# Kernel optimization log

Measured on AMD Instinct MI355X. Metric: run time of the kernel, lower is better.

## Reference

```python
import jax, jax.numpy as jnp
import numpy as np
import math

H, KVH, D = 15, 5, 64  # heads, kv heads, head_dim
ROPE_BASE = 10000.0
NEG = -1e9


def _rope_cos_sin(position_ids):
    # position_ids: [B, S] int -> cos/sin [B, 1, S, D]
    inv_freq = 1.0 / (ROPE_BASE ** (jnp.arange(0, D, 2, dtype=jnp.float32) / D))  # [D/2]
    freqs = position_ids.astype(jnp.float32)[..., None] * inv_freq  # [B, S, D/2]
    emb = jnp.concatenate([freqs, freqs], axis=-1)  # [B, S, D]
    return jnp.cos(emb)[:, None], jnp.sin(emb)[:, None]


def _rotate_half(x):
    x1, x2 = x[..., : D // 2], x[..., D // 2 :]
    return jnp.concatenate([-x2, x1], axis=-1)


def setup_inputs() -> dict:
    key = jax.random.key(0)
    ks = jax.random.split(key, 5)
    B, S, E = 1, 4096, 960
    hidden_states = jax.random.normal(ks[0], (B, S, E), dtype=jnp.float32)
    Wq = jax.random.normal(ks[1], (E, E), dtype=jnp.float32) * 0.02
    Wk = jax.random.normal(ks[2], (KVH * D, E), dtype=jnp.float32) * 0.02
    Wv = jax.random.normal(ks[3], (KVH * D, E), dtype=jnp.float32) * 0.02
    Wo = jax.random.normal(ks[4], (E, E), dtype=jnp.float32) * 0.02
    causal = jnp.tril(jnp.ones((S, S), dtype=bool))
    attention_mask = jnp.where(causal, 0.0, NEG).astype(jnp.float32)[None, None]  # [1,1,S,S]
    position_ids = jnp.arange(S, dtype=jnp.int64 if jax.config.jax_enable_x64 else jnp.int32)[None]
    return {
        "hidden_states": hidden_states,
        "Wq": Wq,
        "Wk": Wk,
        "Wv": Wv,
        "Wo": Wo,
        "attention_mask": attention_mask,
        "position_ids": position_ids,
    }


def reference(hidden_states, Wq, Wk, Wv, Wo, attention_mask, position_ids):
    B, S, E = hidden_states.shape
    groups = H // KVH
    # projections (bias-free Linear: x @ W.T)
    q = (hidden_states @ Wq.T).reshape(B, S, H, D).transpose(0, 2, 1, 3)      # [B,H,S,D]
    k = (hidden_states @ Wk.T).reshape(B, S, KVH, D).transpose(0, 2, 1, 3)    # [B,KVH,S,D]
    v = (hidden_states @ Wv.T).reshape(B, S, KVH, D).transpose(0, 2, 1, 3)    # [B,KVH,S,D]
    cos, sin = _rope_cos_sin(position_ids)  # [B,1,S,D]
    q = q * cos + _rotate_half(q) * sin
    k = k * cos + _rotate_half(k) * sin
    # GQA: repeat_interleave over the head axis
    k = jnp.repeat(k, groups, axis=1)  # [B,H,S,D]
    v = jnp.repeat(v, groups, axis=1)  # [B,H,S,D]
    scores = jnp.einsum("bhqd,bhkd->bhqk", q, k) / math.sqrt(D) + attention_mask
    probs = jax.nn.softmax(scores.astype(jnp.float32), axis=-1).astype(q.dtype)
    out = jnp.einsum("bhqk,bhkd->bhqd", probs, v)  # [B,H,S,D]
    out = out.transpose(0, 2, 1, 3).reshape(B, S, E)
    return out @ Wo.T
```

## Files before the change

kernel.cpp:

```cpp
#include <hip/hip_runtime.h>
#include <hip/hip_bf16.h>

typedef __hip_bfloat16 bf16;
typedef short bf16x8 __attribute__((ext_vector_type(8)));
typedef short bf16x4 __attribute__((ext_vector_type(4)));
typedef float f32x4 __attribute__((ext_vector_type(4)));

static constexpr int S_LEN = 4096;
static constexpr int EMB   = 960;
static constexpr int NH    = 15;
static constexpr int NKVH  = 5;
static constexpr int KV_E  = NKVH * 64;

__device__ __forceinline__ float scrub(float x, float lim) {
  return fminf(fmaxf(x, -lim), lim);
}

__device__ __forceinline__ short f2bf(float x) {
  bf16 h = __float2bfloat16(x);
  short s;
  __builtin_memcpy(&s, &h, 2);
  return s;
}

__device__ __forceinline__ void stage16(const bf16* g, bf16* l) {
  __builtin_amdgcn_global_load_lds(
      (const __attribute__((address_space(1))) void*)g,
      (__attribute__((address_space(3))) void*)l, 16, 0, 0);
}

__global__ void cvt5_kernel(const float* s0, const float* s1, const float* s2,
                            const float* s3, const float* s4,
                            bf16* d0, bf16* d1, bf16* d2, bf16* d3, bf16* d4,
                            int e0, int e1, int e2, int e3, int e4) {
  int i = blockIdx.x * blockDim.x + threadIdx.x;
  const float* s;
  bf16* d;
  int base;
  if (i < e0)      { s = s0; d = d0; base = 0;  }
  else if (i < e1) { s = s1; d = d1; base = e0; }
  else if (i < e2) { s = s2; d = d2; base = e1; }
  else if (i < e3) { s = s3; d = d3; base = e2; }
  else if (i < e4) { s = s4; d = d4; base = e3; }
  else return;
  int k = i - base;
  const float4* sp = (const float4*)s + (size_t)k * 2;
  float4 a = sp[0], b = sp[1];
  bf16x8 r;
  r[0] = f2bf(a.x); r[1] = f2bf(a.y); r[2] = f2bf(a.z); r[3] = f2bf(a.w);
  r[4] = f2bf(b.x); r[5] = f2bf(b.y); r[6] = f2bf(b.z); r[7] = f2bf(b.w);
  *(bf16x8*)((short*)d + (size_t)k * 8) = r;
}

__global__ void zero_kernel(float* __restrict__ p, int n4) {
  int i = blockIdx.x * blockDim.x + threadIdx.x;
  if (i < n4) ((float4*)p)[i] = (float4){0.f, 0.f, 0.f, 0.f};
}

template <typename EPI>
__device__ __forceinline__ void gemm_core(
    const bf16* __restrict__ A, const bf16* __restrict__ W,
    int m0, int n0, int K, bf16* At0, bf16* At1, bf16* Bt0, bf16* Bt1,
    EPI&& epilogue) {
  const int lane = threadIdx.x & 63;
  const int wave = threadIdx.x >> 6;
  const int quad = lane >> 4;
  const int c16  = lane & 15;
  const int wm = wave >> 1, wn = wave & 1;
  const int srow = lane >> 2;
  const int sch  = lane & 3;
  const int NIT  = K / 32;
  bf16* At[2] = {At0, At1};
  bf16* Bt[2] = {Bt0, Bt1};

  auto stage = [&](int b, int k0) {
#pragma unroll
    for (int t = 0; t < 2; t++) {
      int j = wave * 2 + t;
      stage16(A + (size_t)(m0 + j * 16 + srow) * K + k0 + sch * 8,
              At[b] + j * 512);
      stage16(W + (size_t)(n0 + j * 16 + srow) * K + k0 + sch * 8,
              Bt[b] + j * 512);
    }
  };

  f32x4 acc[4][4];
#pragma unroll
  for (int i = 0; i < 4; i++)
#pragma unroll
    for (int j = 0; j < 4; j++) acc[i][j] = (f32x4){0.f, 0.f, 0.f, 0.f};

  stage(0, 0);
  __syncthreads();

  for (int it = 0; it < NIT; ++it) {
    if (it + 1 < NIT) stage((it + 1) & 1, (it + 1) * 32);
    const char* ab = (const char*)At[it & 1];
    const char* bb = (const char*)Bt[it & 1];
    bf16x8 af[4], bfr[4];
#pragma unroll
    for (int i = 0; i < 4; i++)
      af[i] = *(const bf16x8*)(ab + (wm * 64 + i * 16 + c16) * 64 + quad * 16);
#pragma unroll
    for (int j = 0; j < 4; j++)
      bfr[j] = *(const bf16x8*)(bb + (wn * 64 + j * 16 + c16) * 64 + quad * 16);
#pragma unroll
    for (int i = 0; i < 4; i++)
#pragma unroll
      for (int j = 0; j < 4; j++)
        acc[i][j] = __builtin_amdgcn_mfma_f32_16x16x32_bf16(af[i], bfr[j],
                                                            acc[i][j], 0, 0, 0);
    __syncthreads();
  }
  epilogue(acc, m0, n0, wm, wn, quad, c16);
}

__global__ __launch_bounds__(256) void gemm_qkv_kernel(
    const bf16* __restrict__ A, const bf16* __restrict__ Wcat,
    bf16* __restrict__ Qb, bf16* __restrict__ Kbf, bf16* __restrict__ VTb,
    int M, int K) {
  __shared__ __align__(16) bf16 At[2][128 * 32];
  __shared__ __align__(16) bf16 Bt[2][128 * 32];
  const int m0 = blockIdx.x * 128;
  const int n0 = blockIdx.y * 128;
  gemm_core(A, Wcat, m0, n0, K, At[0], At[1], Bt[0], Bt[1],
            [&](f32x4 (&acc)[4][4], int m0_, int n0_, int wm, int wn,
                int quad, int c16) {
#pragma unroll
              for (int i = 0; i < 4; i++)
#pragma unroll
                for (int j = 0; j < 4; j++) {
                  int scol = n0_ + wn * 64 + j * 16;
                  if (scol >= 1600) continue;
                  int colg = scol + c16;
                  int row0 = m0_ + wm * 64 + i * 16 + quad * 4;
                  if (scol < 960) {
#pragma unroll
                    for (int r = 0; r < 4; r++)
                      Qb[(size_t)(row0 + r) * EMB + colg] =
                          __float2bfloat16(scrub(acc[i][j][r], 3e4f));
                  } else if (scol < 1280) {
#pragma unroll
                    for (int r = 0; r < 4; r++)
                      Kbf[(size_t)(row0 + r) * KV_E + (colg - 960)] =
                          __float2bfloat16(scrub(acc[i][j][r], 3e4f));
                  } else {
                    bf16x4 v;
#pragma unroll
                    for (int r = 0; r < 4; r++)
                      v[r] = f2bf(scrub(acc[i][j][r], 3e4f));
                    int t0 = m0_ + wm * 64;
                    int nl = quad * 16 + (i >> 1) * 8 + (i & 1) * 4;
                    *(bf16x4*)((short*)VTb + (size_t)(colg - 1280) * S_LEN +
                               t0 + nl) = v;
                  }
                }
            });
}

__global__ __launch_bounds__(256) void gemm_out_kernel(
    const bf16* __restrict__ A, const bf16* __restrict__ W,
    float* __restrict__ C, int M, int N, int K) {
  __shared__ __align__(16) bf16 At[2][128 * 32];
  __shared__ __align__(16) bf16 Bt[2][128 * 32];
  const int m0 = blockIdx.x * 128;
  const int n0 = blockIdx.y * 128;
  gemm_core(A, W, m0, n0, K, At[0], At[1], Bt[0], Bt[1],
            [&](f32x4 (&acc)[4][4], int m0_, int n0_, int wm, int wn,
                int quad, int c16) {
#pragma unroll
              for (int i = 0; i < 4; i++)
#pragma unroll
                for (int j = 0; j < 4; j++) {
                  int scol = n0_ + wn * 64 + j * 16;
                  if (scol >= EMB) continue;
                  int col = scol + c16;
                  int row0 = m0_ + wm * 64 + i * 16 + quad * 4;
#pragma unroll
                  for (int r = 0; r < 4; r++)
                    C[(size_t)(row0 + r) * EMB + col] =
                        scrub(acc[i][j][r], 3e4f);
                }
            });
}

__global__ void rope2_kernel(bf16* __restrict__ Qb, bf16* __restrict__ Kb,
                             const int* __restrict__ pos_ids) {
  int tid = blockIdx.x * blockDim.x + threadIdx.x;
  if (tid >= S_LEN * (NH + NKVH) * 32) return;
  int d  = tid & 31;
  int hh = (tid >> 5) % (NH + NKVH);
  int s  = tid / ((NH + NKVH) * 32);
  bf16* buf;
  size_t idx;
  float scale;
  if (hh < NH) {
    buf = Qb; idx = (size_t)s * EMB + hh * 64 + d; scale = 0.125f;
  } else {
    buf = Kb; idx = (size_t)s * KV_E + (hh - NH) * 64 + d; scale = 1.0f;
  }
  float x = __bfloat162float(buf[idx]);
  float y = __bfloat162float(buf[idx + 32]);
  float f = (float)pos_ids[s] * expf((float)d * -0.28782313662425572f);
  float sf, cf;
  sincosf(f, &sf, &cf);
  buf[idx]      = __float2bfloat16(scrub((x * cf - y * sf) * scale, 3e4f));
  buf[idx + 32] = __float2bfloat16(scrub((y * cf + x * sf) * scale, 3e4f));
}

__global__ __launch_bounds__(256, 5) void flash_kernel(
    const bf16* __restrict__ Q, const bf16* __restrict__ Kb,
    const bf16* __restrict__ VT, float* __restrict__ Oacc,
    float* __restrict__ Lacc) {
  __shared__ __align__(16) bf16 Kt[2][64 * 64];
  __shared__ __align__(16) bf16 Vt[2][64 * 64];

  const int xq = (int)(gridDim.x - 1) - (int)blockIdx.x;
  const int c  = blockIdx.z;
  if (c > (xq >> 4)) return;

  const int lane = threadIdx.x & 63;
  const int wv   = threadIdx.x >> 6;
  const int quad = lane >> 4;
  const int c16  = lane & 15;
  const int h    = blockIdx.y;
  const int kvh  = h / 3;
  const int qb   = xq * 64;
  const int qw   = qb + wv * 16;
  const int qcol = qw + c16;
  const int it0   = c * 16;
  const int itend = min(it0 + 16, xq + 1);

  const int rsub = lane >> 3;
  const int gch  = (lane & 7) ^ rsub;
  const int rm   = c16 & 7;
  const int ko0  = (quad ^ rm) * 16;

  const bf16* qrow = Q + (size_t)qcol * EMB + h * 64 + quad * 8;
  const bf16x8 aq0 = *(const bf16x8*)qrow;
  const bf16x8 aq1 = *(const bf16x8*)(qrow + 32);

  bf16x4 ones4;
#pragma unroll
  for (int j = 0; j < 4; j++) ones4[j] = (short)0x3F80;

  f32x4 o[4];
#pragma unroll
  for (int n = 0; n < 4; n++) o[n] = (f32x4){0.f, 0.f, 0.f, 0.f};
  f32x4 os = (f32x4){0.f, 0.f, 0.f, 0.f};

  auto stage = [&](int b, int it) {
    const int kbase = it * 64;
#pragma unroll
    for (int t = 0; t < 2; t++) {
      int i = wv * 2 + t;
      int r = i * 8 + rsub;
      stage16(Kb + (size_t)(kbase + r) * KV_E + kvh * 64 + gch * 8,
              &Kt[b][i * 512]);
      stage16(VT + (size_t)(kvh * 64 + r) * S_LEN + kbase + gch * 8,
              &Vt[b][i * 512]);
    }
  };

  stage(0, it0);
  __syncthreads();

  for (int it = it0; it < itend; ++it) {
    if (it + 1 < itend) stage((it + 1) & 1, it + 1);

    const int kbase = it * 64;
    const char* kb = (const char*)&Kt[it & 1][0];
    const char* vb = (const char*)&Vt[it & 1][0];
    const bool masked = (it == xq);

    bf16x4 pp[4];
#pragma unroll
    for (int cc = 0; cc < 4; cc++) {
      int r = cc * 16 + c16;
      bf16x8 b0 = *(const bf16x8*)(kb + r * 128 + ko0);
      bf16x8 b1 = *(const bf16x8*)(kb + r * 128 + (ko0 ^ 64));
      f32x4 s = (f32x4){0.f, 0.f, 0.f, 0.f};
      s = __builtin_amdgcn_mfma_f32_16x16x32_bf16(b0, aq0, s, 0, 0, 0);
      s = __builtin_amdgcn_mfma_f32_16x16x32_bf16(b1, aq1, s, 0, 0, 0);
#pragma unroll
      for (int r4 = 0; r4 < 4; r4++) {
        float p = __expf(fminf(s[r4], 80.f));
        if (masked) {
          int kc = kbase + cc * 16 + quad * 4 + r4;
          p = (kc <= qcol) ? p : 0.f;
        }
        pp[cc][r4] = f2bf(p);
      }
    }

#pragma unroll
    for (int cc = 0; cc < 4; cc++)
      os = __builtin_amdgcn_mfma_f32_16x16x16bf16_1k(ones4, pp[cc], os,
                                                     0, 0, 0);

#pragma unroll
    for (int n = 0; n < 4; n++) {
      const char* vrow = vb + (n * 16 + c16) * 128;
#pragma unroll
      for (int ccp = 0; ccp < 2; ccp++) {
        int m = quad * 2 + ccp;
        bf16x8 vv = *(const bf16x8*)(vrow + ((m ^ rm) * 16));
        bf16x4 vlo = __builtin_shufflevector(vv, vv, 0, 1, 2, 3);
        bf16x4 vhi = __builtin_shufflevector(vv, vv, 4, 5, 6, 7);
        o[n] = __builtin_amdgcn_mfma_f32_16x16x16bf16_1k(vlo, pp[ccp * 2],
                                                         o[n], 0, 0, 0);
        o[n] = __builtin_amdgcn_mfma_f32_16x16x16bf16_1k(vhi, pp[ccp * 2 + 1],
                                                         o[n], 0, 0, 0);
      }
    }

    __syncthreads();
  }

  if (quad == 0)
    atomicAdd(&Lacc[(size_t)(qw + c16) * NH + h], os[0]);

  float* zone = (float*)((char*)&Kt[0][0] + wv * 1280 * 4);
#pragma unroll
  for (int n = 0; n < 4; n++) {
    *(f32x4*)(zone + c16 * 20 + quad * 4) = o[n];
    asm volatile("s_waitcnt lgkmcnt(0)" ::: "memory");
#pragma unroll
    for (int r = 0; r < 4; r++) {
      float t = zone[(quad * 4 + r) * 20 + c16];
      atomicAdd(&Oacc[(size_t)(qw + quad * 4 + r) * EMB + h * 64 + n * 16 +
                      c16], t);
    }
    asm volatile("" ::: "memory");
  }
}

__global__ void normalize_kernel(const float* __restrict__ Oacc,
                                 const float* __restrict__ Lacc,
                                 bf16* __restrict__ O) {
  int i = blockIdx.x * blockDim.x + threadIdx.x;
  if (i >= S_LEN * (EMB / 4)) return;
  int row = i / (EMB / 4);
  int col = (i % (EMB / 4)) * 4;
  int h = col >> 6;
  float l = fmaxf(Lacc[(size_t)row * NH + h], 1e-20f);
  float4 v = *(const float4*)&Oacc[(size_t)row * EMB + col];
  bf16x4 r;
  r[0] = f2bf(scrub(v.x / l, 1e4f));
  r[1] = f2bf(scrub(v.y / l, 1e4f));
  r[2] = f2bf(scrub(v.z / l, 1e4f));
  r[3] = f2bf(scrub(v.w / l, 1e4f));
  *(bf16x4*)((short*)O + (size_t)row * EMB + col) = r;
}

extern "C" void kernel_launch(void* const* d_in, const int* in_sizes, int n_in,
                              void* d_out, int out_size, void* d_ws, size_t ws_size,
                              hipStream_t stream) {
  const float* hs = (const float*)d_in[0];
  const float* Wq = (const float*)d_in[1];
  const float* Wk = (const float*)d_in[2];
  const float* Wv = (const float*)d_in[3];
  const float* Wo = (const float*)d_in[4];
  const int* pos = (const int*)d_in[6];
  float* out = (float*)d_out;

  char* wsb = (char*)d_ws;
  float* Oacc = (float*)wsb;
  float* Lacc = Oacc + (size_t)S_LEN * EMB;
  size_t regA = ((size_t)S_LEN * EMB + (size_t)S_LEN * NH) * sizeof(float);
  bf16* hsb = (bf16*)wsb;
  bf16* Qb  = (bf16*)(wsb + regA);
  bf16* Kbf = Qb + (size_t)S_LEN * EMB;
  bf16* VTb = Kbf + (size_t)S_LEN * KV_E;
  bf16* Wqb = VTb + (size_t)S_LEN * KV_E;
  bf16* Wkb = Wqb + (size_t)EMB * EMB;
  bf16* Wvb = Wkb + (size_t)KV_E * EMB;
  bf16* Wob = Wqb + (size_t)1664 * EMB;

  {
    int e0 = (S_LEN * EMB) / 8;
    int e1 = e0 + (EMB * EMB) / 8;
    int e2 = e1 + (KV_E * EMB) / 8;
    int e3 = e2 + (KV_E * EMB) / 8;
    int e4 = e3 + (EMB * EMB) / 8;
    cvt5_kernel<<<(e4 + 255) / 256, 256, 0, stream>>>(
        hs, Wq, Wk, Wv, Wo, hsb, Wqb, Wkb, Wvb, Wob, e0, e1, e2, e3, e4);
  }

  gemm_qkv_kernel<<<dim3(S_LEN / 128, 13), 256, 0, stream>>>(
      hsb, Wqb, Qb, Kbf, VTb, S_LEN, EMB);

  {
    int n = S_LEN * (NH + NKVH) * 32;
    rope2_kernel<<<(n + 255) / 256, 256, 0, stream>>>(Qb, Kbf, pos);
  }

  {
    int n4 = (S_LEN * EMB + S_LEN * NH) / 4;
    zero_kernel<<<(n4 + 255) / 256, 256, 0, stream>>>(Oacc, n4);
  }
  flash_kernel<<<dim3(S_LEN / 64, NH, 4), 256, 0, stream>>>(Qb, Kbf, VTb,
                                                            Oacc, Lacc);
  {
    int n = S_LEN * (EMB / 4);
    normalize_kernel<<<(n + 255) / 256, 256, 0, stream>>>(Oacc, Lacc, Qb);
  }

  gemm_out_kernel<<<dim3(S_LEN / 128, 8), 256, 0, stream>>>(
      Qb, Wob, out, S_LEN, EMB, EMB);
}
```

Before: 278.6 us.

## Drop split-KV atomics, normalize in flash kernel, use exp2 with folded scale

Removes the 4-way split over the KV axis together with its zeroing, float atomic accumulation and separate normalize kernel. Each block now walks the whole causal KV range and writes the normalized bf16 output in place over Q. The Q scale now folds in log2(e) so the softmax can use exp2f without the clamp. The V transpose layout is permuted so the PV MFMA can reuse the same swizzled load pattern as K. The cost is fewer blocks and a longer serial loop for late query tiles, which risks load imbalance, plus an in-place write to Q that relies on each block reading only its own Q rows.

```diff
diff --git a/kernel.cpp b/kernel.cpp
--- a/kernel.cpp
+++ b/kernel.cpp
@@ -52,11 +52,6 @@
   *(bf16x8*)((short*)d + (size_t)k * 8) = r;
 }
 
-__global__ void zero_kernel(float* __restrict__ p, int n4) {
-  int i = blockIdx.x * blockDim.x + threadIdx.x;
-  if (i < n4) ((float4*)p)[i] = (float4){0.f, 0.f, 0.f, 0.f};
-}
-
 template <typename EPI>
 __device__ __forceinline__ void gemm_core(
     const bf16* __restrict__ A, const bf16* __restrict__ W,
@@ -150,7 +145,7 @@
                     for (int r = 0; r < 4; r++)
                       v[r] = f2bf(scrub(acc[i][j][r], 3e4f));
                     int t0 = m0_ + wm * 64;
-                    int nl = quad * 16 + (i >> 1) * 8 + (i & 1) * 4;
+                    int nl = quad * 8 + (i >> 1) * 32 + (i & 1) * 4;
                     *(bf16x4*)((short*)VTb + (size_t)(colg - 1280) * S_LEN +
                                t0 + nl) = v;
                   }
@@ -195,7 +190,8 @@
   size_t idx;
   float scale;
   if (hh < NH) {
-    buf = Qb; idx = (size_t)s * EMB + hh * 64 + d; scale = 0.125f;
+    buf = Qb; idx = (size_t)s * EMB + hh * 64 + d;
+    scale = 0.18033688011112042f;
   } else {
     buf = Kb; idx = (size_t)s * KV_E + (hh - NH) * 64 + d; scale = 1.0f;
   }
@@ -209,15 +205,12 @@
 }
 
 __global__ __launch_bounds__(256, 5) void flash_kernel(
-    const bf16* __restrict__ Q, const bf16* __restrict__ Kb,
-    const bf16* __restrict__ VT, float* __restrict__ Oacc,
-    float* __restrict__ Lacc) {
+    const bf16* Q, const bf16* __restrict__ Kb,
+    const bf16* __restrict__ VT, bf16* O) {
   __shared__ __align__(16) bf16 Kt[2][64 * 64];
   __shared__ __align__(16) bf16 Vt[2][64 * 64];
 
   const int xq = (int)(gridDim.x - 1) - (int)blockIdx.x;
-  const int c  = blockIdx.z;
-  if (c > (xq >> 4)) return;
 
   const int lane = threadIdx.x & 63;
   const int wv   = threadIdx.x >> 6;
@@ -228,8 +221,7 @@
   const int qb   = xq * 64;
   const int qw   = qb + wv * 16;
   const int qcol = qw + c16;
-  const int it0   = c * 16;
-  const int itend = min(it0 + 16, xq + 1);
+  const int itend = xq + 1;
 
   const int rsub = lane >> 3;
   const int gch  = (lane & 7) ^ rsub;
@@ -262,10 +254,10 @@
     }
   };
 
-  stage(0, it0);
+  stage(0, 0);
   __syncthreads();
 
-  for (int it = it0; it < itend; ++it) {
+  for (int it = 0; it < itend; ++it) {
     if (it + 1 < itend) stage((it + 1) & 1, it + 1);
 
     const int kbase = it * 64;
@@ -284,7 +276,7 @@
       s = __builtin_amdgcn_mfma_f32_16x16x32_bf16(b1, aq1, s, 0, 0, 0);
 #pragma unroll
       for (int r4 = 0; r4 < 4; r4++) {
-        float p = __expf(fminf(s[r4], 80.f));
+        float p = exp2f(s[r4]);
         if (masked) {
           int kc = kbase + cc * 16 + quad * 4 + r4;
           p = (kc <= qcol) ? p : 0.f;
@@ -301,56 +293,31 @@
 #pragma unroll
     for (int n = 0; n < 4; n++) {
       const char* vrow = vb + (n * 16 + c16) * 128;
-#pragma unroll
-      for (int ccp = 0; ccp < 2; ccp++) {
-        int m = quad * 2 + ccp;
-        bf16x8 vv = *(const bf16x8*)(vrow + ((m ^ rm) * 16));
-        bf16x4 vlo = __builtin_shufflevector(vv, vv, 0, 1, 2, 3);
-        bf16x4 vhi = __builtin_shufflevector(vv, vv, 4, 5, 6, 7);
-        o[n] = __builtin_amdgcn_mfma_f32_16x16x16bf16_1k(vlo, pp[ccp * 2],
-                                                         o[n], 0, 0, 0);
-        o[n] = __builtin_amdgcn_mfma_f32_16x16x16bf16_1k(vhi, pp[ccp * 2 + 1],
-                                                         o[n], 0, 0, 0);
-      }
+      bf16x8 va = *(const bf16x8*)(vrow + ko0);
+      bf16x8 vc = *(const bf16x8*)(vrow + (ko0 ^ 64));
+      bf16x4 a0 = __builtin_shufflevector(va, va, 0, 1, 2, 3);
+      bf16x4 a1 = __builtin_shufflevector(va, va, 4, 5, 6, 7);
+      bf16x4 a2 = __builtin_shufflevector(vc, vc, 0, 1, 2, 3);
+      bf16x4 a3 = __builtin_shufflevector(vc, vc, 4, 5, 6, 7);
+      o[n] = __builtin_amdgcn_mfma_f32_16x16x16bf16_1k(a0, pp[0], o[n], 0, 0, 0);
+      o[n] = __builtin_amdgcn_mfma_f32_16x16x16bf16_1k(a1, pp[1], o[n], 0, 0, 0);
+      o[n] = __builtin_amdgcn_mfma_f32_16x16x16bf16_1k(a2, pp[2], o[n], 0, 0, 0);
+      o[n] = __builtin_amdgcn_mfma_f32_16x16x16bf16_1k(a3, pp[3], o[n], 0, 0, 0);
     }
 
     __syncthreads();
   }
 
-  if (quad == 0)
-    atomicAdd(&Lacc[(size_t)(qw + c16) * NH + h], os[0]);
-
-  float* zone = (float*)((char*)&Kt[0][0] + wv * 1280 * 4);
+  const float inv = 1.0f / fmaxf(os[0], 1e-20f);
 #pragma unroll
   for (int n = 0; n < 4; n++) {
-    *(f32x4*)(zone + c16 * 20 + quad * 4) = o[n];
-    asm volatile("s_waitcnt lgkmcnt(0)" ::: "memory");
-#pragma unroll
-    for (int r = 0; r < 4; r++) {
-      float t = zone[(quad * 4 + r) * 20 + c16];
-      atomicAdd(&Oacc[(size_t)(qw + quad * 4 + r) * EMB + h * 64 + n * 16 +
-                      c16], t);
-    }
-    asm volatile("" ::: "memory");
-  }
-}
-
-__global__ void normalize_kernel(const float* __restrict__ Oacc,
-                                 const float* __restrict__ Lacc,
-                                 bf16* __restrict__ O) {
-  int i = blockIdx.x * blockDim.x + threadIdx.x;
-  if (i >= S_LEN * (EMB / 4)) return;
-  int row = i / (EMB / 4);
-  int col = (i % (EMB / 4)) * 4;
-  int h = col >> 6;
-  float l = fmaxf(Lacc[(size_t)row * NH + h], 1e-20f);
-  float4 v = *(const float4*)&Oacc[(size_t)row * EMB + col];
-  bf16x4 r;
-  r[0] = f2bf(scrub(v.x / l, 1e4f));
-  r[1] = f2bf(scrub(v.y / l, 1e4f));
-  r[2] = f2bf(scrub(v.z / l, 1e4f));
-  r[3] = f2bf(scrub(v.w / l, 1e4f));
-  *(bf16x4*)((short*)O + (size_t)row * EMB + col) = r;
+    bf16x4 w;
+#pragma unroll
+    for (int r = 0; r < 4; r++)
+      w[r] = f2bf(scrub(o[n][r] * inv, 1e4f));
+    *(bf16x4*)((short*)O + (size_t)qcol * EMB + h * 64 + n * 16 + quad * 4) =
+        w;
+  }
 }
 
 extern "C" void kernel_launch(void* const* d_in, const int* in_sizes, int n_in,
@@ -365,8 +332,6 @@
   float* out = (float*)d_out;
 
   char* wsb = (char*)d_ws;
-  float* Oacc = (float*)wsb;
-  float* Lacc = Oacc + (size_t)S_LEN * EMB;
   size_t regA = ((size_t)S_LEN * EMB + (size_t)S_LEN * NH) * sizeof(float);
   bf16* hsb = (bf16*)wsb;
   bf16* Qb  = (bf16*)(wsb + regA);
@@ -395,16 +360,7 @@
     rope2_kernel<<<(n + 255) / 256, 256, 0, stream>>>(Qb, Kbf, pos);
   }
 
-  {
-    int n4 = (S_LEN * EMB + S_LEN * NH) / 4;
-    zero_kernel<<<(n4 + 255) / 256, 256, 0, stream>>>(Oacc, n4);
-  }
-  flash_kernel<<<dim3(S_LEN / 64, NH, 4), 256, 0, stream>>>(Qb, Kbf, VTb,
-                                                            Oacc, Lacc);
-  {
-    int n = S_LEN * (EMB / 4);
-    normalize_kernel<<<(n + 255) / 256, 256, 0, stream>>>(Oacc, Lacc, Qb);
-  }
+  flash_kernel<<<dim3(S_LEN / 64, NH), 256, 0, stream>>>(Qb, Kbf, VTb, Qb);
 
   gemm_out_kernel<<<dim3(S_LEN / 128, 8), 256, 0, stream>>>(
       Qb, Wob, out, S_LEN, EMB, EMB);
```

Measured after the change: 281.0 us. About the same (+0.9%).
